# Optimization experiments

Measured on AMD Instinct MI355X. Metric: run time of the kernel, lower is better.

Reference implementation:

```python
import jax, jax.numpy as jnp
import numpy as np

N, B = 128, 8                                # seq_len, batch
V, E, H, S, T = 32000, 256, 256, 256, 32     # vocab, embed, hidden, segment_dim, segment_threshold


def _gru_cell(x, h, Wi, Wh, bi, bh):
    # PyTorch GRU cell convention (gates ordered r,z,n)
    gi = x @ Wi.T + bi
    gh = h @ Wh.T + bh
    ir, iz, inn = jnp.split(gi, 3, axis=-1)
    hr, hz, hn = jnp.split(gh, 3, axis=-1)
    r = jax.nn.sigmoid(ir + hr)
    z = jax.nn.sigmoid(iz + hz)
    n = jnp.tanh(inn + r * hn)
    return (1.0 - z) * n + z * h


def _run_gru(xs, h0, Wi, Wh, bi, bh):
    def step(h, x):
        h = _gru_cell(x, h, Wi, Wh, bi, bh)
        return h, h
    hT, ys = jax.lax.scan(step, h0, xs)
    return ys, hT


def setup_inputs() -> dict:
    key = jax.random.key(0)
    ks = jax.random.split(key, 17)
    sc = 1.0 / np.sqrt(H).astype(np.float32)
    w = lambda k, shape: jax.random.normal(k, shape, jnp.float32) * sc
    return {
        "tokens": jax.random.randint(ks[0], (N, B), 0, V, dtype=jnp.int32),
        "emb": w(ks[1], (V, E)),
        "Wi_f": w(ks[2], (3 * H, E)), "Wh_f": w(ks[3], (3 * H, H)),
        "bi_f": w(ks[4], (3 * H,)),  "bh_f": w(ks[5], (3 * H,)),
        "Wi_r": w(ks[6], (3 * H, E)), "Wh_r": w(ks[7], (3 * H, H)),
        "bi_r": w(ks[8], (3 * H,)),  "bh_r": w(ks[9], (3 * H,)),
        "Wi_s": w(ks[10], (3 * S, 2 * H)), "Wh_s": w(ks[11], (3 * S, S)),
        "bi_s": w(ks[12], (3 * S,)), "bh_s": w(ks[13], (3 * S,)),
        # deterministic stand-ins for the per-start torch.randn initial hiddens
        "h0f": jax.random.normal(ks[14], (N, B, S), jnp.float32),
        "h0b": jax.random.normal(ks[15], (N, B, S), jnp.float32),
    }


def reference(tokens, emb, Wi_f, Wh_f, bi_f, bh_f, Wi_r, Wh_r, bi_r, bh_r,
              Wi_s, Wh_s, bi_s, bh_s, h0f, h0b):
    x = emb[tokens]                                   # (N,B,E); dropout p=0
    h0 = jnp.zeros((B, H), x.dtype)
    ys_f, _ = _run_gru(x, h0, Wi_f, Wh_f, bi_f, bh_f)
    ys_r, _ = _run_gru(x[::-1], h0, Wi_r, Wh_r, bi_r, bh_r)
    outputs = jnp.concatenate([ys_f, ys_r[::-1]], axis=-1)   # (N,B,2H)

    def seg(window, h0i):                             # window (T,B,2H)
        def step(h, xt):
            h = _gru_cell(xt, h, Wi_s, Wh_s, bi_s, bh_s)
            return h, h
        hT, ys = jax.lax.scan(step, h0i, window)
        return ys, hT

    ii = jnp.arange(N)[:, None]                       # (N,1) segment start i
    tt = jnp.arange(T)[None, :]                       # (1,T) step within window
    jf = ii + tt                                      # forward target column j
    jb = ii - tt                                      # backward target row j
    win_f = outputs[jnp.clip(jf, 0, N - 1)]           # (N,T,B,2H)
    win_b = outputs[jnp.clip(jb, 0, N - 1)]
    outs_f, _ = jax.vmap(seg)(win_f, h0f)             # (N,T,B,S)
    outs_b, hT_b = jax.vmap(seg)(win_b, h0b)

    jf_s = jnp.where(jf < N, jf, N)                   # OOB index -> dropped
    jb_s = jnp.where(jb >= 0, jb, N)
    dp_f = jnp.zeros((N, N, B, S), outputs.dtype).at[ii, jf_s].set(outs_f, mode="drop")
    dp_b = jnp.zeros((N, N, B, S), outputs.dtype).at[jb_s, ii].set(outs_b, mode="drop")
    dp = jnp.concatenate([dp_f, dp_b], axis=-1)       # (N,N,B,2S)
    rows, cols = jnp.triu_indices(N)
    dp_tri = dp[rows, cols]                           # (N*(N+1)/2, B, 2S)

    # final hiddens as the torch loops leave them: forward i=N-1 runs exactly
    # one step; backward i=N-1 runs T steps (N >= T so all in range).
    hid_f = _gru_cell(outputs[-1], h0f[-1], Wi_s, Wh_s, bi_s, bh_s)
    hidden = jnp.concatenate([hid_f, hT_b[-1]], axis=-1)[None]  # (1,B,2S)
    return dp_tri, hidden
```

## Files before the change

### kernel.cpp

```cpp
#include <hip/hip_runtime.h>
#include <cstdint>
#include <cstddef>

#define NN 128
#define BB 8
#define EE 256
#define HH 256
#define SS 256
#define TT 32
#define G3 768
#define HBSTR 264
#define HIDOFF 33816576ull
#define OUT_ELEMS 33820672ull

typedef __attribute__((ext_vector_type(8))) short bf16x8;
typedef __attribute__((ext_vector_type(4))) float f32x4;
typedef _Float16 f16;
typedef __attribute__((ext_vector_type(2))) _Float16 f16x2;

__device__ __forceinline__ float bf2f(unsigned short u) {
    union { unsigned u; float f; } v; v.u = ((unsigned)u) << 16; return v.f;
}
__device__ __forceinline__ unsigned short f2bf(float f) {
    union { float f; unsigned u; } v; v.f = f;
    unsigned r = v.u + 0x7fffu + ((v.u >> 16) & 1u);
    return (unsigned short)(r >> 16);
}
__device__ __forceinline__ unsigned short f2h(float f) {
    union { f16 h; unsigned short u; } v; v.h = (f16)f; return v.u;
}
__device__ __forceinline__ float dot2h(unsigned wu, unsigned hu, float acc) {
    union { unsigned u; f16x2 h; } a, b2;
    a.u = wu; b2.u = hu;
    return __builtin_amdgcn_fdot2(a.h, b2.h, acc, false);
}
__device__ __forceinline__ float rcpf(float x) { return __builtin_amdgcn_rcpf(x); }
__device__ __forceinline__ float sigm(float x) { return rcpf(1.f + __expf(-x)); }
__device__ __forceinline__ float tanh_fast(float x) {
    float xc = fminf(fmaxf(x, -10.f), 10.f);
    float e2 = __expf(2.f * xc);
    return (e2 - 1.f) * rcpf(e2 + 1.f);
}

__device__ __forceinline__ int detect_f32(const void* emb) {
    const unsigned* w = (const unsigned*)emb;
    int bad = 0;
    for (int i = 0; i < 128; ++i) {
        unsigned u = w[i];
        bad |= (((u >> 7)  & 0xFFu) >= 0xC8u);
        bad |= (((u >> 23) & 0xFFu) >= 0xC8u);
    }
    return bad;
}
__device__ __forceinline__ float lds1(const void* p, size_t i, int f32) {
    return f32 ? ((const float*)p)[i] : bf2f(((const unsigned short*)p)[i]);
}
__device__ __forceinline__ void outw(void* p, size_t i, float v, int f32) {
    if (f32) ((float*)p)[i] = v;
    else ((unsigned short*)p)[i] = f2bf(v);
}

__global__ __launch_bounds__(256) void conv_all(
    const void* __restrict__ Wi_f, const void* __restrict__ Wi_r,
    const void* __restrict__ Wh_f, const void* __restrict__ Wh_r,
    const void* __restrict__ Wh_s, const void* __restrict__ Wi_s,
    unsigned short* __restrict__ dst, const void* __restrict__ emb) {
    const int f32 = detect_f32(emb);
    size_t i = ((size_t)blockIdx.x * 256 + threadIdx.x) * 8;
    const void* src; size_t off; int h16 = 0;
    if      (i < 196608)  { src = Wi_f; off = i; }
    else if (i < 393216)  { src = Wi_r; off = i - 196608; }
    else if (i < 589824)  { src = Wh_f; off = i - 393216; h16 = 1; }
    else if (i < 786432)  { src = Wh_r; off = i - 589824; h16 = 1; }
    else if (i < 983040)  { src = Wh_s; off = i - 786432; }
    else                  { src = Wi_s; off = i - 983040; }
    bf16x8 v;
    if (f32) {
        const float* q = (const float*)src + off;
        float4 a = *(const float4*)q, b4 = *(const float4*)(q + 4);
        float f[8] = {a.x, a.y, a.z, a.w, b4.x, b4.y, b4.z, b4.w};
#pragma unroll
        for (int j = 0; j < 8; ++j)
            v[j] = (short)(h16 ? f2h(f[j]) : f2bf(f[j]));
    } else {
        v = *(const bf16x8*)((const unsigned short*)src + off);
        if (h16) {
#pragma unroll
            for (int j = 0; j < 8; ++j)
                v[j] = (short)f2h(bf2f((unsigned short)v[j]));
        }
    }
    *(bf16x8*)(dst + i) = v;
}

template <int KK>
__global__ __launch_bounds__(256) void gemm_mfma(
    const int* __restrict__ tok, const void* __restrict__ Asrc,
    const unsigned short* __restrict__ W,  const void* __restrict__ bias,
    unsigned short* __restrict__ C,
    const unsigned short* __restrict__ W2, const void* __restrict__ bias2,
    unsigned short* __restrict__ C2, const void* __restrict__ emb) {

    const int f32 = detect_f32(emb);
    __shared__ unsigned short As[64 * 260];

    int bid = blockIdx.x;
    const unsigned short* Wp = W; const void* bp = bias; unsigned short* Cp = C;
    if (C2 && bid >= 128) { bid -= 128; Wp = W2; bp = bias2; Cp = C2; }
    const int mb = bid >> 3, nb = bid & 7;

    const int tid = threadIdx.x, wave = tid >> 6, lane = tid & 63;
    const int l15 = lane & 15, quad = lane >> 4;

    f32x4 acc[6];
#pragma unroll
    for (int nt = 0; nt < 6; ++nt) acc[nt] = (f32x4){0.f, 0.f, 0.f, 0.f};

    for (int kh = 0; kh < KK; kh += 256) {
        __syncthreads();
        for (int e = tid * 4; e < 64 * 256; e += 1024) {
            int r = e >> 8, k = e & 255;
            int gr = mb * 64 + r;
            unsigned short h4[4];
            if (tok) {
                size_t arow = (size_t)tok[gr] * EE + kh + k;
                if (f32) {
                    float4 v = *(const float4*)((const float*)Asrc + arow);
                    h4[0] = f2bf(v.x); h4[1] = f2bf(v.y); h4[2] = f2bf(v.z); h4[3] = f2bf(v.w);
                } else {
                    *(uint2*)h4 = *(const uint2*)((const unsigned short*)Asrc + arow);
                }
            } else {
                *(uint2*)h4 = *(const uint2*)((const unsigned short*)Asrc + (size_t)gr * KK + kh + k);
            }
            *(uint2*)(As + r * 260 + k) = *(uint2*)h4;
        }
        __syncthreads();
#pragma unroll
        for (int kt = 0; kt < 8; ++kt) {
            bf16x8 Af = *(const bf16x8*)(As + (wave * 16 + l15) * 260 + kt * 32 + quad * 8);
#pragma unroll
            for (int nt = 0; nt < 6; ++nt) {
                int col = nb * 96 + nt * 16 + l15;
                bf16x8 Bfr = *(const bf16x8*)(Wp + (size_t)col * KK + kh + kt * 32 + quad * 8);
                acc[nt] = __builtin_amdgcn_mfma_f32_16x16x32_bf16(Af, Bfr, acc[nt], 0, 0, 0);
            }
        }
    }
#pragma unroll
    for (int nt = 0; nt < 6; ++nt) {
        int col = nb * 96 + nt * 16 + l15;
        float bv = lds1(bp, col, f32);
#pragma unroll
        for (int r4 = 0; r4 < 4; ++r4) {
            int row = mb * 64 + wave * 16 + quad * 4 + r4;
            Cp[(size_t)row * G3 + col] = f2bf(acc[nt][r4] + bv);
        }
    }
}

#define LOAD_BFRAGS(Whc)                                                        \
    bf16x8 Ba[8][8]; bf16x8 Bv[8][4];                                           \
    _Pragma("unroll")                                                           \
    for (int nt = 0; nt < 12; ++nt) {                                           \
        int col = wave * 192 + nt * 16 + l15;                                   \
        _Pragma("unroll")                                                       \
        for (int kt = 0; kt < 8; ++kt) {                                        \
            bf16x8 f = *(const bf16x8*)(Whc + (size_t)col * 256 + kt * 32 + quad * 8); \
            if (nt < 8) Ba[kt][nt] = f; else Bv[kt][nt - 8] = f;                \
        }                                                                       \
    }                                                                           \
    _Pragma("unroll")                                                           \
    for (int kt = 0; kt < 8; ++kt) {                                            \
        _Pragma("unroll")                                                       \
        for (int nt = 0; nt < 8; ++nt) asm volatile("" : "+a"(Ba[kt][nt]));     \
        _Pragma("unroll")                                                       \
        for (int nt = 0; nt < 4; ++nt) asm volatile("" : "+v"(Bv[kt][nt]));     \
    }

#define MFMA_GH()                                                               \
    {                                                                           \
        f32x4 acc[12];                                                          \
        _Pragma("unroll")                                                       \
        for (int nt = 0; nt < 12; ++nt) acc[nt] = (f32x4){0.f, 0.f, 0.f, 0.f};  \
        _Pragma("unroll")                                                       \
        for (int kt = 0; kt < 8; ++kt) {                                        \
            bf16x8 Af = *(const bf16x8*)(hb + l15 * HBSTR + kt * 32 + quad * 8);\
            _Pragma("unroll")                                                   \
            for (int nt = 0; nt < 8; ++nt)                                      \
                acc[nt] = __builtin_amdgcn_mfma_f32_16x16x32_bf16(Af, Ba[kt][nt], acc[nt], 0, 0, 0); \
            _Pragma("unroll")                                                   \
            for (int nt = 0; nt < 4; ++nt)                                      \
                acc[8 + nt] = __builtin_amdgcn_mfma_f32_16x16x32_bf16(Af, Bv[kt][nt], acc[8 + nt], 0, 0, 0); \
        }                                                                       \
        if (quad < 2) {                                                         \
            _Pragma("unroll")                                                   \
            for (int nt = 0; nt < 12; ++nt) {                                   \
                int col = wave * 192 + nt * 16 + l15;                           \
                _Pragma("unroll")                                               \
                for (int r4 = 0; r4 < 4; ++r4) gh[quad * 4 + r4][col] = acc[nt][r4]; \
            }                                                                   \
        }                                                                       \
    }

__global__ __attribute__((amdgpu_flat_work_group_size(512, 512), amdgpu_waves_per_eu(2, 2)))
void token_scan_zero(
    const unsigned short* __restrict__ gi_f, const unsigned short* __restrict__ gi_r,
    const unsigned short* __restrict__ Wh_fh, const unsigned short* __restrict__ Wh_rh,
    const void* __restrict__ bh_f, const void* __restrict__ bh_r,
    unsigned short* __restrict__ outp, void* __restrict__ dout,
    const void* __restrict__ emb) {

    const int f32 = detect_f32(emb);

    if (blockIdx.x >= 16) {
        uint4 z = {0u, 0u, 0u, 0u};
        uint4* p = (uint4*)dout;
        const size_t nvec = OUT_ELEMS * (f32 ? 4 : 2) / 16;
        size_t stride = (size_t)(gridDim.x - 16) * 512;
        for (size_t v = (size_t)(blockIdx.x - 16) * 512 + threadIdx.x; v < nvec; v += stride)
            p[v] = z;
        return;
    }

    const int dir = blockIdx.x & 1;
    const int b   = blockIdx.x >> 1;
    const int tid = threadIdx.x;
    const int c = tid & 255, kh = tid >> 8;

    __shared__ __align__(16) unsigned short hbs[256];
    __shared__ float pr[3][256];

    const unsigned short* Wh = dir ? Wh_rh : Wh_fh;
    const unsigned short* gi = dir ? gi_r : gi_f;
    const void* bh = dir ? bh_r : bh_f;

    unsigned w[192];
#pragma unroll
    for (int g = 0; g < 3; ++g) {
        const unsigned* wp = (const unsigned*)(Wh + (size_t)(g * 256 + c) * 256 + kh * 128);
#pragma unroll
        for (int q = 0; q < 16; ++q) {
            uint4 v = *(const uint4*)(wp + q * 4);
            w[g * 64 + q * 4 + 0] = v.x; w[g * 64 + q * 4 + 1] = v.y;
            w[g * 64 + q * 4 + 2] = v.z; w[g * 64 + q * 4 + 3] = v.w;
        }
    }
    const float bh0 = lds1(bh, c, f32);
    const float bh1 = lds1(bh, c + 256, f32);
    const float bh2 = lds1(bh, c + 512, f32);

    if (tid < 256) hbs[tid] = 0;
    float hreg = 0.f;
    __syncthreads();

    const unsigned* hbw = (const unsigned*)hbs + kh * 64;
    for (int t = 0; t < NN; ++t) {
        const int row = dir ? (NN - 1 - t) : t;
        unsigned short g0 = 0, g1 = 0, g2 = 0;
        if (kh == 0) {
            const unsigned short* gp = gi + (size_t)row * BB * G3 + (size_t)b * G3;
            g0 = gp[c]; g1 = gp[c + 256]; g2 = gp[c + 512];
        }
        float a0 = 0.f, a1 = 0.f, a2 = 0.f;
#pragma unroll
        for (int q = 0; q < 16; ++q) {
            uint4 hv = *(const uint4*)(hbw + q * 4);
            a0 = dot2h(w[      q * 4 + 0], hv.x, a0);
            a0 = dot2h(w[      q * 4 + 1], hv.y, a0);
            a0 = dot2h(w[      q * 4 + 2], hv.z, a0);
            a0 = dot2h(w[      q * 4 + 3], hv.w, a0);
            a1 = dot2h(w[ 64 + q * 4 + 0], hv.x, a1);
            a1 = dot2h(w[ 64 + q * 4 + 1], hv.y, a1);
            a1 = dot2h(w[ 64 + q * 4 + 2], hv.z, a1);
            a1 = dot2h(w[ 64 + q * 4 + 3], hv.w, a1);
            a2 = dot2h(w[128 + q * 4 + 0], hv.x, a2);
            a2 = dot2h(w[128 + q * 4 + 1], hv.y, a2);
            a2 = dot2h(w[128 + q * 4 + 2], hv.z, a2);
            a2 = dot2h(w[128 + q * 4 + 3], hv.w, a2);
        }
        if (kh) { pr[0][c] = a0; pr[1][c] = a1; pr[2][c] = a2; }
        __syncthreads();
        if (kh == 0) {
            a0 += pr[0][c]; a1 += pr[1][c]; a2 += pr[2][c];
            float rr = sigm(bf2f(g0) + a0 + bh0);
            float zz = sigm(bf2f(g1) + a1 + bh1);
            float nn = tanh_fast(bf2f(g2) + rr * (a2 + bh2));
            float hn = (1.f - zz) * nn + zz * hreg;
            hreg = hn;
            hbs[c] = f2h(hn);
        }
        __syncthreads();
        if (kh == 0)
            outp[((size_t)(row * BB + b)) * 512 + dir * 256 + c] = f2bf(hreg);
    }
}

__global__ __attribute__((amdgpu_flat_work_group_size(256, 256), amdgpu_waves_per_eu(1, 1)))
void seg_scan(
    const unsigned short* __restrict__ gi,
    const unsigned short* __restrict__ Whc,
    const void* __restrict__ bh,
    const void* __restrict__ h0f, const void* __restrict__ h0b,
    void* __restrict__ dout, const void* __restrict__ emb) {

    const int f32 = detect_f32(emb);

    __shared__ float gh[BB][G3];
    __shared__ __align__(16) unsigned short hb[16 * HBSTR];

    const int tid = threadIdx.x;
    const int wave = tid >> 6, lane = tid & 63;
    const int l15 = lane & 15, quad = lane >> 4;
    const int dir = blockIdx.x & 1, i0 = blockIdx.x >> 1;

    LOAD_BFRAGS(Whc)

    const void* h0 = dir ? h0b : h0f;
    const size_t h0base = (size_t)i0 * (BB * SS);
    const int c = tid;
    const float bh0 = lds1(bh, c, f32);
    const float bh1 = lds1(bh, c + 256, f32);
    const float bh2 = lds1(bh, c + 512, f32);
    float hreg[BB];
#pragma unroll
    for (int b = 0; b < BB; ++b) {
        float v = lds1(h0, h0base + b * 256 + c, f32);
        hreg[b] = v;
        hb[b * HBSTR + c] = f2bf(v);
    }
    for (int e = 8 * HBSTR + tid; e < 16 * HBSTR; e += 256) hb[e] = 0;
    __syncthreads();

    const int nsteps = dir ? min(TT, i0 + 1) : min(TT, NN - i0);
    for (int t = 0; t < nsteps; ++t) {
        const int j = dir ? (i0 - t) : (i0 + t);
        unsigned short gpre[BB][3];
        const unsigned short* gp = gi + (size_t)j * BB * G3;
#pragma unroll
        for (int b = 0; b < BB; ++b) {
            gpre[b][0] = gp[b * G3 + c];
            gpre[b][1] = gp[b * G3 + c + 256];
            gpre[b][2] = gp[b * G3 + c + 512];
        }
        MFMA_GH()
        __syncthreads();

#pragma unroll
        for (int b = 0; b < BB; ++b) {
            float rr = sigm(bf2f(gpre[b][0]) + gh[b][c] + bh0);
            float zz = sigm(bf2f(gpre[b][1]) + gh[b][c + 256] + bh1);
            float nn = tanh_fast(bf2f(gpre[b][2]) + rr * (gh[b][c + 512] + bh2));
            float hn = (1.f - zz) * nn + zz * hreg[b];
            hreg[b] = hn;
            hb[b * HBSTR + c] = f2bf(hn);
        }
        __syncthreads();

        const int r0 = dir ? j : i0;
        const size_t tri = (size_t)r0 * NN - (size_t)(r0 * (r0 - 1)) / 2 + t;
        const size_t obase = tri * (BB * 512) + (dir ? 256 : 0);
#pragma unroll
        for (int b = 0; b < BB; ++b) {
            outw(dout, obase + b * 512 + c, hreg[b], f32);
            if (i0 == NN - 1) {
                if (dir == 0 && t == 0)      outw(dout, HIDOFF + b * 512 + c, hreg[b], f32);
                if (dir == 1 && t == TT - 1) outw(dout, HIDOFF + 256 + b * 512 + c, hreg[b], f32);
            }
        }
    }
}

extern "C" void kernel_launch(void* const* d_in, const int* in_sizes, int n_in,
                              void* d_out, int out_size, void* d_ws, size_t ws_size,
                              hipStream_t stream) {
    const int* tokens = (const int*)d_in[0];
    const void* emb   = d_in[1];
    const void* Wi_f  = d_in[2];
    const void* Wh_f  = d_in[3];
    const void* bi_f  = d_in[4];
    const void* bh_f  = d_in[5];
    const void* Wi_r  = d_in[6];
    const void* Wh_r  = d_in[7];
    const void* bi_r  = d_in[8];
    const void* bh_r  = d_in[9];
    const void* Wi_s  = d_in[10];
    const void* Wh_s  = d_in[11];
    const void* bi_s  = d_in[12];
    const void* bh_s  = d_in[13];
    const void* h0f   = d_in[14];
    const void* h0b   = d_in[15];

    unsigned short* wsu = (unsigned short*)d_ws;
    unsigned short* gif  = wsu;
    unsigned short* gir  = wsu + 786432;
    unsigned short* outp = wsu + 1572864;
    unsigned short* wcv  = wsu + 2097152;
    unsigned short* gis  = gif;

    const unsigned short* Wi_fc = wcv;
    const unsigned short* Wi_rc = wcv + 196608;
    const unsigned short* Wh_fh = wcv + 393216;
    const unsigned short* Wh_rh = wcv + 589824;
    const unsigned short* Wh_sc = wcv + 786432;
    const unsigned short* Wi_sc = wcv + 983040;

    conv_all<<<dim3(672), dim3(256), 0, stream>>>(Wi_f, Wi_r, Wh_f, Wh_r, Wh_s, Wi_s,
                                                  wcv, emb);
    gemm_mfma<256><<<dim3(256), dim3(256), 0, stream>>>(
        tokens, emb, Wi_fc, bi_f, gif, Wi_rc, bi_r, gir, emb);
    token_scan_zero<<<dim3(256), dim3(512), 0, stream>>>(gif, gir, Wh_fh, Wh_rh,
                                                         bh_f, bh_r, outp, d_out, emb);
    gemm_mfma<512><<<dim3(128), dim3(256), 0, stream>>>(
        nullptr, outp, Wi_sc, bi_s, gis, nullptr, nullptr, nullptr, emb);
    seg_scan<<<dim3(256), dim3(256), 0, stream>>>(gis, Wh_sc, bh_s, h0f, h0b, d_out, emb);
}
```

Measured before the change: 501.6 us.

## Split seg_scan across 8 waves and pin token_scan weights in VGPRs

The segment GRU scan kernel goes from 4 to 8 waves per block. Each wave now holds 6 column tiles of the recurrent weight in registers instead of 12, and the gate update is split so each half of the block handles 4 batch rows. This halves the serial MFMA chain per wave on every step, at the cost of lower register budget per wave (waves_per_eu 2) and more threads in each barrier. The token scan also gets asm barriers that keep its weight array resident in VGPRs rather than letting the compiler spill or reload it.

Result: slower. 539.0 us (+7.5%).

```diff
diff --git a/kernel.cpp b/kernel.cpp
--- a/kernel.cpp
+++ b/kernel.cpp
@@ -159,50 +159,6 @@
     }
 }
 
-#define LOAD_BFRAGS(Whc)                                                        \
-    bf16x8 Ba[8][8]; bf16x8 Bv[8][4];                                           \
-    _Pragma("unroll")                                                           \
-    for (int nt = 0; nt < 12; ++nt) {                                           \
-        int col = wave * 192 + nt * 16 + l15;                                   \
-        _Pragma("unroll")                                                       \
-        for (int kt = 0; kt < 8; ++kt) {                                        \
-            bf16x8 f = *(const bf16x8*)(Whc + (size_t)col * 256 + kt * 32 + quad * 8); \
-            if (nt < 8) Ba[kt][nt] = f; else Bv[kt][nt - 8] = f;                \
-        }                                                                       \
-    }                                                                           \
-    _Pragma("unroll")                                                           \
-    for (int kt = 0; kt < 8; ++kt) {                                            \
-        _Pragma("unroll")                                                       \
-        for (int nt = 0; nt < 8; ++nt) asm volatile("" : "+a"(Ba[kt][nt]));     \
-        _Pragma("unroll")                                                       \
-        for (int nt = 0; nt < 4; ++nt) asm volatile("" : "+v"(Bv[kt][nt]));     \
-    }
-
-#define MFMA_GH()                                                               \
-    {                                                                           \
-        f32x4 acc[12];                                                          \
-        _Pragma("unroll")                                                       \
-        for (int nt = 0; nt < 12; ++nt) acc[nt] = (f32x4){0.f, 0.f, 0.f, 0.f};  \
-        _Pragma("unroll")                                                       \
-        for (int kt = 0; kt < 8; ++kt) {                                        \
-            bf16x8 Af = *(const bf16x8*)(hb + l15 * HBSTR + kt * 32 + quad * 8);\
-            _Pragma("unroll")                                                   \
-            for (int nt = 0; nt < 8; ++nt)                                      \
-                acc[nt] = __builtin_amdgcn_mfma_f32_16x16x32_bf16(Af, Ba[kt][nt], acc[nt], 0, 0, 0); \
-            _Pragma("unroll")                                                   \
-            for (int nt = 0; nt < 4; ++nt)                                      \
-                acc[8 + nt] = __builtin_amdgcn_mfma_f32_16x16x32_bf16(Af, Bv[kt][nt], acc[8 + nt], 0, 0, 0); \
-        }                                                                       \
-        if (quad < 2) {                                                         \
-            _Pragma("unroll")                                                   \
-            for (int nt = 0; nt < 12; ++nt) {                                   \
-                int col = wave * 192 + nt * 16 + l15;                           \
-                _Pragma("unroll")                                               \
-                for (int r4 = 0; r4 < 4; ++r4) gh[quad * 4 + r4][col] = acc[nt][r4]; \
-            }                                                                   \
-        }                                                                       \
-    }
-
 __global__ __attribute__((amdgpu_flat_work_group_size(512, 512), amdgpu_waves_per_eu(2, 2)))
 void token_scan_zero(
     const unsigned short* __restrict__ gi_f, const unsigned short* __restrict__ gi_r,
@@ -246,6 +202,9 @@
             w[g * 64 + q * 4 + 2] = v.z; w[g * 64 + q * 4 + 3] = v.w;
         }
     }
+#pragma unroll
+    for (int i = 0; i < 192; ++i) asm volatile("" : "+v"(w[i]));
+
     const float bh0 = lds1(bh, c, f32);
     const float bh1 = lds1(bh, c + 256, f32);
     const float bh2 = lds1(bh, c + 512, f32);
@@ -296,7 +255,7 @@
     }
 }
 
-__global__ __attribute__((amdgpu_flat_work_group_size(256, 256), amdgpu_waves_per_eu(1, 1)))
+__global__ __attribute__((amdgpu_flat_work_group_size(512, 512), amdgpu_waves_per_eu(2, 2)))
 void seg_scan(
     const unsigned short* __restrict__ gi,
     const unsigned short* __restrict__ Whc,
@@ -314,45 +273,79 @@
     const int l15 = lane & 15, quad = lane >> 4;
     const int dir = blockIdx.x & 1, i0 = blockIdx.x >> 1;
 
-    LOAD_BFRAGS(Whc)
+    bf16x8 Ba[8][6];
+#pragma unroll
+    for (int nt = 0; nt < 6; ++nt) {
+        int col = wave * 96 + nt * 16 + l15;
+#pragma unroll
+        for (int kt = 0; kt < 8; ++kt)
+            Ba[kt][nt] = *(const bf16x8*)(Whc + (size_t)col * 256 + kt * 32 + quad * 8);
+    }
+#pragma unroll
+    for (int kt = 0; kt < 8; ++kt)
+#pragma unroll
+        for (int nt = 0; nt < 6; ++nt) asm volatile("" : "+a"(Ba[kt][nt]));
 
     const void* h0 = dir ? h0b : h0f;
     const size_t h0base = (size_t)i0 * (BB * SS);
-    const int c = tid;
+    const int c = tid & 255;
+    const int half = tid >> 8;
     const float bh0 = lds1(bh, c, f32);
     const float bh1 = lds1(bh, c + 256, f32);
     const float bh2 = lds1(bh, c + 512, f32);
-    float hreg[BB];
-#pragma unroll
-    for (int b = 0; b < BB; ++b) {
+    float hreg[4];
+#pragma unroll
+    for (int q = 0; q < 4; ++q) {
+        int b = half * 4 + q;
         float v = lds1(h0, h0base + b * 256 + c, f32);
-        hreg[b] = v;
+        hreg[q] = v;
         hb[b * HBSTR + c] = f2bf(v);
     }
-    for (int e = 8 * HBSTR + tid; e < 16 * HBSTR; e += 256) hb[e] = 0;
+    for (int e = 8 * HBSTR + tid; e < 16 * HBSTR; e += 512) hb[e] = 0;
     __syncthreads();
 
     const int nsteps = dir ? min(TT, i0 + 1) : min(TT, NN - i0);
     for (int t = 0; t < nsteps; ++t) {
         const int j = dir ? (i0 - t) : (i0 + t);
-        unsigned short gpre[BB][3];
+        unsigned short gpre[4][3];
         const unsigned short* gp = gi + (size_t)j * BB * G3;
 #pragma unroll
-        for (int b = 0; b < BB; ++b) {
-            gpre[b][0] = gp[b * G3 + c];
-            gpre[b][1] = gp[b * G3 + c + 256];
-            gpre[b][2] = gp[b * G3 + c + 512];
-        }
-        MFMA_GH()
-        __syncthreads();
-
-#pragma unroll
-        for (int b = 0; b < BB; ++b) {
-            float rr = sigm(bf2f(gpre[b][0]) + gh[b][c] + bh0);
-            float zz = sigm(bf2f(gpre[b][1]) + gh[b][c + 256] + bh1);
-            float nn = tanh_fast(bf2f(gpre[b][2]) + rr * (gh[b][c + 512] + bh2));
-            float hn = (1.f - zz) * nn + zz * hreg[b];
-            hreg[b] = hn;
+        for (int q = 0; q < 4; ++q) {
+            int b = half * 4 + q;
+            gpre[q][0] = gp[b * G3 + c];
+            gpre[q][1] = gp[b * G3 + c + 256];
+            gpre[q][2] = gp[b * G3 + c + 512];
+        }
+        {
+            f32x4 acc[6];
+#pragma unroll
+            for (int nt = 0; nt < 6; ++nt) acc[nt] = (f32x4){0.f, 0.f, 0.f, 0.f};
+#pragma unroll
+            for (int kt = 0; kt < 8; ++kt) {
+                bf16x8 Af = *(const bf16x8*)(hb + l15 * HBSTR + kt * 32 + quad * 8);
+#pragma unroll
+                for (int nt = 0; nt < 6; ++nt)
+                    acc[nt] = __builtin_amdgcn_mfma_f32_16x16x32_bf16(Af, Ba[kt][nt], acc[nt], 0, 0, 0);
+            }
+            if (quad < 2) {
+#pragma unroll
+                for (int nt = 0; nt < 6; ++nt) {
+                    int col = wave * 96 + nt * 16 + l15;
+#pragma unroll
+                    for (int r4 = 0; r4 < 4; ++r4) gh[quad * 4 + r4][col] = acc[nt][r4];
+                }
+            }
+        }
+        __syncthreads();
+
+#pragma unroll
+        for (int q = 0; q < 4; ++q) {
+            int b = half * 4 + q;
+            float rr = sigm(bf2f(gpre[q][0]) + gh[b][c] + bh0);
+            float zz = sigm(bf2f(gpre[q][1]) + gh[b][c + 256] + bh1);
+            float nn = tanh_fast(bf2f(gpre[q][2]) + rr * (gh[b][c + 512] + bh2));
+            float hn = (1.f - zz) * nn + zz * hreg[q];
+            hreg[q] = hn;
             hb[b * HBSTR + c] = f2bf(hn);
         }
         __syncthreads();
@@ -361,11 +354,12 @@
         const size_t tri = (size_t)r0 * NN - (size_t)(r0 * (r0 - 1)) / 2 + t;
         const size_t obase = tri * (BB * 512) + (dir ? 256 : 0);
 #pragma unroll
-        for (int b = 0; b < BB; ++b) {
-            outw(dout, obase + b * 512 + c, hreg[b], f32);
+        for (int q = 0; q < 4; ++q) {
+            int b = half * 4 + q;
+            outw(dout, obase + b * 512 + c, hreg[q], f32);
             if (i0 == NN - 1) {
-                if (dir == 0 && t == 0)      outw(dout, HIDOFF + b * 512 + c, hreg[b], f32);
-                if (dir == 1 && t == TT - 1) outw(dout, HIDOFF + 256 + b * 512 + c, hreg[b], f32);
+                if (dir == 0 && t == 0)      outw(dout, HIDOFF + b * 512 + c, hreg[q], f32);
+                if (dir == 1 && t == TT - 1) outw(dout, HIDOFF + 256 + b * 512 + c, hreg[q], f32);
             }
         }
     }
@@ -413,5 +407,5 @@
                                                          bh_f, bh_r, outp, d_out, emb);
     gemm_mfma<512><<<dim3(128), dim3(256), 0, stream>>>(
         nullptr, outp, Wi_sc, bi_s, gis, nullptr, nullptr, nullptr, emb);
-    seg_scan<<<dim3(256), dim3(256), 0, stream>>>(gis, Wh_sc, bh_s, h0f, h0b, d_out, emb);
-}
+    seg_scan<<<dim3(256), dim3(512), 0, stream>>>(gis, Wh_sc, bh_s, h0f, h0b, d_out, emb);
+}
```
